# Performance work log

Measured on AMD Instinct MI355X. Metric: run time of the kernel, lower is better.

Reference implementation:

```python
import jax, jax.numpy as jnp
import numpy as np

N, M, C = 16384, 4096, 32
R = 2.0            # max_neighbour_distance
MULT = 2.0         # neighbor_distance_multiplier
NV = 3             # voxels per axis
TV = NV * NV * NV  # 27 total grid voxels
CH = 128           # query chunk size for kNN
EPS_D = 1e-8
BN_EPS = 1e-5


def _grid_offsets():
    g = jnp.linspace(-R + R / NV, R - R / NV, NV)
    x, y, z = jnp.meshgrid(g, g, g, indexing='ij')
    return jnp.stack([x.ravel(), y.ravel(), z.ravel()], axis=-1)  # (27,3)


def _three_nn(support_xyz, new_xyz, grid_centers):
    """3-NN of each grid center among support points within a cube of half-width
    MULT*R around the parent keypoint (two-step search, neighbor_type=0 cube).
    Returns squared dists (M,27,3), idx (M,27,3), empty (M,)."""
    q = new_xyz.reshape(-1, CH, 3)
    g = grid_centers.reshape(-1, CH, TV, 3)

    def body(args):
        qc, gc = args                                   # (CH,3), (CH,27,3)
        diff = jnp.abs(support_xyz[None, :, :] - qc[:, None, :])   # (CH,N,3)
        cand = jnp.max(diff, axis=-1) <= MULT * R                   # (CH,N)
        d2 = jnp.sum((gc[:, :, None, :] - support_xyz[None, None, :, :]) ** 2,
                     axis=-1)                                       # (CH,27,N)
        d2 = jnp.where(cand[:, None, :], d2, jnp.inf)
        nd, idx = jax.lax.top_k(-d2, 3)                              # (CH,27,3)
        return -nd, idx, ~jnp.any(cand, axis=-1)

    d3, idx, empty = jax.lax.map(body, (q, g))
    d3 = jnp.where(jnp.isinf(d3), 1e10, d3)  # <3 candidates -> ~zero weight
    return (d3.reshape(-1, TV, 3), idx.reshape(-1, TV, 3), empty.reshape(-1))


def _bn_relu(x, gamma, beta):
    mu = jnp.mean(x, axis=0)
    var = jnp.var(x, axis=0)
    return jax.nn.relu((x - mu) * jax.lax.rsqrt(var + BN_EPS) * gamma + beta)


def _forward(support_xyz, support_features, new_xyz,
             w1, bn1_gamma, bn1_beta, w2, bn2_gamma, bn2_beta):
    grid_centers = new_xyz[:, None, :] + _grid_offsets()[None, :, :]  # (M,27,3)
    d3, idx, empty = _three_nn(support_xyz, new_xyz, grid_centers)
    d3 = jax.lax.stop_gradient(d3)  # torch computes kNN under no_grad

    dist_recip = 1.0 / (d3 + EPS_D)                                   # (M,27,3)
    norm = jnp.sum(dist_recip, axis=-1, keepdims=True)
    weight = dist_recip / jnp.maximum(norm, 1e-8)

    nbr_feats = support_features[idx]                 # (M,27,3,C) gather
    interp = jnp.einsum('mgk,mgkc->mgc', weight, nbr_feats)          # (M,27,C)

    nbr_xyz = support_xyz[idx]                        # (M,27,3,3)
    local_xyz = (grid_centers[:, :, None, :] - nbr_xyz).reshape(M, TV, 9)
    feats = jnp.concatenate([interp, local_xyz], axis=-1)            # (M,27,C+9)
    feats = jnp.where(empty[:, None, None], 0.0, feats)

    # grouped Conv1d (kernel 1, groups=27): per-voxel matmul
    y = jnp.einsum('mgc,goc->mgo', feats, w1).reshape(M, TV * 32)     # (M,864)
    y = _bn_relu(y, bn1_gamma, bn1_beta)
    z = y @ w2.T                                                      # (M,128)
    return _bn_relu(z, bn2_gamma, bn2_beta)


def setup_inputs() -> dict:
    key = jax.random.key(0)
    ks = jax.random.split(key, 5)
    scale = jnp.array([50.0, 50.0, 4.0])
    shift = jnp.array([0.0, 0.0, -2.0])
    support_xyz = jax.random.uniform(ks[0], (N, 3)) * scale + shift
    new_xyz = jax.random.uniform(ks[1], (M, 3)) * scale + shift
    support_features = jax.random.normal(ks[2], (N, C))
    w1 = jax.random.normal(ks[3], (TV, 32, C + 9)) * (2.0 / (C + 9)) ** 0.5
    w2 = jax.random.normal(ks[4], (128, TV * 32)) * (2.0 / (TV * 32)) ** 0.5
    return {
        'support_xyz': support_xyz,
        'support_features': support_features,
        'new_xyz': new_xyz,
        'w1': w1,
        'bn1_gamma': jnp.ones(TV * 32),
        'bn1_beta': jnp.zeros(TV * 32),
        'w2': w2,
        'bn2_gamma': jnp.ones(128),
        'bn2_beta': jnp.zeros(128),
    }


def reference(support_xyz, support_features, new_xyz,
              w1, bn1_gamma, bn1_beta, w2, bn2_gamma, bn2_beta):
    return _forward(support_xyz, support_features, new_xyz,
                    w1, bn1_gamma, bn1_beta, w2, bn2_gamma, bn2_beta)
```

## Files before the change

### kernel.cpp

```cpp
#include <hip/hip_runtime.h>
#include <hip/hip_bf16.h>

#define N_SUP 16384
#define M_Q   4096
#define TV    27
#define CIN   41
#define CH1   864
#define CH2   128
#define CAP   1024
#define NB    12

#define KC_BK  24
#define KC_KS  216
#define KC_NCH 4

__device__ __forceinline__ float gsel(int i){
  const float GOFF = (float)(-2.0 + 2.0 / 3.0);
  return (i == 0) ? GOFF : ((i == 2) ? -GOFF : 0.0f);
}

__device__ __forceinline__ int binOf(float x){
  int b = (int)(x * (float)(NB / 50.0));
  return (b < 0) ? 0 : ((b > NB - 1) ? NB - 1 : b);
}

__device__ __forceinline__ void insK(unsigned long long key,
                                     unsigned long long& k0,
                                     unsigned long long& k1,
                                     unsigned long long& k2){
  bool b0 = key < k0, b1 = key < k1, b2 = key < k2;
  k2 = b1 ? k1 : (b2 ? key : k2);
  k1 = b0 ? k0 : (b1 ? key : k1);
  k0 = b0 ? key : k0;
}

__global__ void kPre(const float* __restrict__ w1, float* __restrict__ w1T,
                     const float* __restrict__ w2, float* __restrict__ w2T,
                     const float* __restrict__ sup_xyz, int* __restrict__ counts)
{
  int idx = blockIdx.x * 256 + threadIdx.x;
  if (idx < N_SUP) {
    float x = sup_xyz[3*idx], y = sup_xyz[3*idx+1];
    atomicAdd(&counts[binOf(x) * NB + binOf(y)], 1);
  }
  if (idx < CIN * CH1) {
    int k = idx / CH1, t = idx % CH1;
    w1T[idx] = w1[(size_t)t * CIN + k];
  }
  int j = idx - CIN * CH1;
  if (j >= 0 && j < CH1 * CH2) {
    int k = j / CH2, c = j % CH2;
    w2T[j] = w2[(size_t)c * CH1 + k];
  }
}

__global__ void kScan(const int* __restrict__ counts, int* __restrict__ starts, int* __restrict__ cursor)
{
  __shared__ int sc[NB*NB];
  int t = threadIdx.x;
  if (t < NB*NB) sc[t] = counts[t];
  __syncthreads();
  if (t == 0) {
    int acc = 0;
    for (int b = 0; b < NB*NB; b++) { int c = sc[b]; sc[b] = acc; acc += c; }
  }
  __syncthreads();
  if (t < NB*NB) { starts[t] = sc[t]; cursor[t] = sc[t]; }
  if (t == NB*NB) starts[NB*NB] = N_SUP;
}

__global__ void kScatter(const float* __restrict__ sup_xyz, int* __restrict__ cursor,
                         float* __restrict__ xs, float* __restrict__ ys,
                         float* __restrict__ zs, int* __restrict__ sid)
{
  int i = blockIdx.x * 256 + threadIdx.x;
  if (i < N_SUP) {
    float x = sup_xyz[3*i], y = sup_xyz[3*i+1], z = sup_xyz[3*i+2];
    int b = binOf(x) * NB + binOf(y);
    int p = atomicAdd(&cursor[b], 1);
    xs[p] = x; ys[p] = y; zs[p] = z; sid[p] = i;
  }
}

__global__ __launch_bounds__(256) void kA12(const float* __restrict__ xs,
                                            const float* __restrict__ ys,
                                            const float* __restrict__ zs,
                                            const int*   __restrict__ sid,
                                            const int*   __restrict__ starts,
                                            const float* __restrict__ new_xyz,
                                            const float* __restrict__ sup_xyz,
                                            float* __restrict__ nnW,
                                            int*   __restrict__ nnGI,
                                            float* __restrict__ nnLX)
{
  __shared__ float4 cxyz[CAP];
  __shared__ unsigned long long sk[TV][8][3];
  __shared__ int s_cnt;

  const int m   = blockIdx.x;
  const int tid = threadIdx.x;
  if (tid == 0) s_cnt = 0;
  __syncthreads();

  const float qx = new_xyz[m*3+0];
  const float qy = new_xyz[m*3+1];
  const float qz = new_xyz[m*3+2];

  const int bx0 = binOf(qx - 4.0f), bx1 = binOf(qx + 4.0f);
  const int by0 = binOf(qy - 4.0f), by1 = binOf(qy + 4.0f);
  for (int bx = bx0; bx <= bx1; bx++) {
    const int beg = starts[bx * NB + by0];
    const int end = starts[bx * NB + by1 + 1];
    for (int i = beg + tid; i < end; i += 256) {
      float x = xs[i], y = ys[i];
      if (fabsf(__fsub_rn(x, qx)) <= 4.0f && fabsf(__fsub_rn(y, qy)) <= 4.0f) {
        int p = atomicAdd(&s_cnt, 1);
        if (p < CAP) cxyz[p] = make_float4(x, y, zs[i], __uint_as_float((unsigned)sid[i]));
      }
    }
  }
  __syncthreads();
  const int cnt = (s_cnt < CAP) ? s_cnt : CAP;

  const int v = tid >> 3, j = tid & 7;
  if (v < TV) {
    const float gx = qx + gsel(v / 9);
    const float gy = qy + gsel((v / 3) % 3);
    const float gz = qz + gsel(v % 3);
    unsigned long long k0 = ~0ull, k1 = ~0ull, k2 = ~0ull;
    float k2df = __uint_as_float(0xFFFFFFFFu);
    for (int c = j; c < cnt; c += 8) {
      float4 f4 = cxyz[c];
      float dx = __fsub_rn(gx, f4.x);
      float dy = __fsub_rn(gy, f4.y);
      float dz = __fsub_rn(gz, f4.z);
      float dd = __fadd_rn(__fadd_rn(__fmul_rn(dx,dx), __fmul_rn(dy,dy)), __fmul_rn(dz,dz));
      if (!(dd > k2df)) {
        unsigned long long key = ((unsigned long long)__float_as_uint(dd) << 32)
                               | (unsigned long long)__float_as_uint(f4.w);
        insK(key, k0, k1, k2);
        k2df = __uint_as_float((unsigned)(k2 >> 32));
      }
    }
    sk[v][j][0] = k0; sk[v][j][1] = k1; sk[v][j][2] = k2;
  }
  __syncthreads();

  if (tid < TV) {
    const int vv = tid;
    const float gx = qx + gsel(vv / 9);
    const float gy = qy + gsel((vv / 3) % 3);
    const float gz = qz + gsel(vv % 3);
    unsigned long long k0 = ~0ull, k1 = ~0ull, k2 = ~0ull;
    #pragma unroll
    for (int jj = 0; jj < 8; jj++) {
      insK(sk[vv][jj][0], k0, k1, k2);
      insK(sk[vv][jj][1], k0, k1, k2);
      insK(sk[vv][jj][2], k0, k1, k2);
    }
    const int base = m * TV + vv;
    if (cnt > 0) {
      unsigned long long ks[3] = {k0, k1, k2};
      float d[3]; int gi[3]; bool ok[3];
      #pragma unroll
      for (int r = 0; r < 3; r++) {
        unsigned db = (unsigned)(ks[r] >> 32);
        ok[r] = (db != 0xFFFFFFFFu);
        d[r]  = ok[r] ? __uint_as_float(db) : 1e10f;
        gi[r] = ok[r] ? (int)(unsigned)(ks[r] & 0xFFFFFFFFull) : 0;
      }
      float r0 = 1.0f / (d[0] + 1e-8f);
      float r1 = 1.0f / (d[1] + 1e-8f);
      float r2 = 1.0f / (d[2] + 1e-8f);
      float den = fmaxf(r0 + r1 + r2, 1e-8f);
      nnW[base*3+0] = r0 / den; nnW[base*3+1] = r1 / den; nnW[base*3+2] = r2 / den;
      nnGI[base*3+0] = gi[0]; nnGI[base*3+1] = gi[1]; nnGI[base*3+2] = gi[2];
      #pragma unroll
      for (int r = 0; r < 3; r++) {
        if (ok[r]) {
          nnLX[base*9 + r*3 + 0] = gx - sup_xyz[gi[r]*3 + 0];
          nnLX[base*9 + r*3 + 1] = gy - sup_xyz[gi[r]*3 + 1];
          nnLX[base*9 + r*3 + 2] = gz - sup_xyz[gi[r]*3 + 2];
        } else {
          nnLX[base*9 + r*3 + 0] = 0.0f;
          nnLX[base*9 + r*3 + 1] = 0.0f;
          nnLX[base*9 + r*3 + 2] = 0.0f;
        }
      }
    } else {
      #pragma unroll
      for (int r = 0; r < 3; r++) {
        nnW[base*3+r] = 0.0f; nnGI[base*3+r] = 0;
        nnLX[base*9+r*3+0] = 0.0f; nnLX[base*9+r*3+1] = 0.0f; nnLX[base*9+r*3+2] = 0.0f;
      }
    }
  }
}

__global__ __launch_bounds__(256) void kA3(const float* __restrict__ sup_feat,
                                           const float* __restrict__ nnW,
                                           const int*   __restrict__ nnGI,
                                           const float* __restrict__ nnLX,
                                           const float* __restrict__ w1T,
                                           float* __restrict__ y1,
                                           float* __restrict__ stats1)
{
  __shared__ float s_feats[8][TV][CIN];
  __shared__ float s_w[8][TV][3];
  __shared__ int   s_gi[8][TV][3];

  const int m0  = blockIdx.x * 8;
  const int tid = threadIdx.x;

  for (int t = tid; t < 8*TV*3; t += 256) {
    int q = t / (TV*3), rem = t % (TV*3);
    s_w[q][rem/3][rem%3]  = nnW[m0*TV*3 + t];
    s_gi[q][rem/3][rem%3] = nnGI[m0*TV*3 + t];
  }
  for (int t = tid; t < 8*TV*9; t += 256) {
    int q = t / (TV*9), rem = t % (TV*9);
    s_feats[q][rem/9][32 + rem%9] = nnLX[m0*TV*9 + t];
  }
  __syncthreads();

  for (int t = tid; t < 8*TV*32; t += 256) {
    const int q = t / (TV*32), rem = t % (TV*32);
    const int v = rem >> 5, ch = rem & 31;
    s_feats[q][v][ch] = s_w[q][v][0] * sup_feat[s_gi[q][v][0]*32 + ch]
                      + s_w[q][v][1] * sup_feat[s_gi[q][v][1]*32 + ch]
                      + s_w[q][v][2] * sup_feat[s_gi[q][v][2]*32 + ch];
  }
  __syncthreads();

  const int copy = (blockIdx.x & 7) * 2 * CH1;
  for (int t = tid; t < CH1; t += 256) {
    const int v = t >> 5;
    float acc[8];
    #pragma unroll
    for (int q = 0; q < 8; q++) acc[q] = 0.0f;
    for (int k = 0; k < CIN; k++) {
      float w = w1T[k * CH1 + t];
      #pragma unroll
      for (int q = 0; q < 8; q++) acc[q] += s_feats[q][v][k] * w;
    }
    float s = 0.0f, ss = 0.0f;
    #pragma unroll
    for (int q = 0; q < 8; q++) {
      y1[(size_t)(m0 + q) * CH1 + t] = acc[q];
      s += acc[q]; ss += acc[q] * acc[q];
    }
    atomicAdd(&stats1[copy + t],       s);
    atomicAdd(&stats1[copy + CH1 + t], ss);
  }
}

__global__ void kS(const float* __restrict__ stats1,
                   const float* __restrict__ g1, const float* __restrict__ b1,
                   float* __restrict__ scsg, float* __restrict__ shsg)
{
  int c = blockIdx.x * 256 + threadIdx.x;
  if (c < CH1) {
    float s = 0.0f, ssq = 0.0f;
    #pragma unroll
    for (int k = 0; k < 8; k++) {
      s   += stats1[k * 2 * CH1 + c];
      ssq += stats1[k * 2 * CH1 + CH1 + c];
    }
    float mu  = s  * (1.0f / M_Q);
    float var = ssq * (1.0f / M_Q) - mu * mu;
    float r   = 1.0f / sqrtf(var + 1e-5f);
    float gg = g1[c];
    scsg[c] = r * gg;
    shsg[c] = b1[c] - mu * r * gg;
  }
}

__global__ __launch_bounds__(256) void kC(const float* __restrict__ y1,
                                          const float* __restrict__ scsg,
                                          const float* __restrict__ shsg,
                                          const float* __restrict__ w2T,
                                          float* __restrict__ zpart)
{
  __shared__ float As[KC_BK][36];
  __shared__ float Bs[KC_BK][CH2];
  __shared__ float lsc[KC_KS], lsh[KC_KS];

  const int tid = threadIdx.x;
  const int mb  = blockIdx.x & 127;
  const int ch  = blockIdx.x >> 7;
  const int m0  = mb * 32;
  const int kb  = ch * KC_KS;

  for (int t = tid; t < KC_KS; t += 256) { lsc[t] = scsg[kb + t]; lsh[t] = shsg[kb + t]; }

  const int ar = tid >> 3;
  const int ac = (tid & 7) * 3;
  const int ty = tid >> 5;
  const int tx = tid & 31;

  float pa0, pa1, pa2; float4 pb[3];
  {
    const float* yr = &y1[(size_t)(m0 + ar) * CH1 + kb + ac];
    pa0 = yr[0]; pa1 = yr[1]; pa2 = yr[2];
    #pragma unroll
    for (int jj = 0; jj < 3; jj++) {
      int fid = tid + jj * 256; int kk = fid >> 5, c4 = (fid & 31) * 4;
      pb[jj] = *(const float4*)&w2T[(size_t)(kb + kk) * CH2 + c4];
    }
  }

  float acc[4][4];
  #pragma unroll
  for (int i = 0; i < 4; i++)
    #pragma unroll
    for (int jj = 0; jj < 4; jj++) acc[i][jj] = 0.0f;

  for (int kt = 0; kt < KC_KS / KC_BK; kt++) {
    __syncthreads();
    const int kl = kt * KC_BK + ac;
    As[ac  ][ar] = fmaxf(pa0 * lsc[kl  ] + lsh[kl  ], 0.0f);
    As[ac+1][ar] = fmaxf(pa1 * lsc[kl+1] + lsh[kl+1], 0.0f);
    As[ac+2][ar] = fmaxf(pa2 * lsc[kl+2] + lsh[kl+2], 0.0f);
    #pragma unroll
    for (int jj = 0; jj < 3; jj++) {
      int fid = tid + jj * 256; int kk = fid >> 5, c4 = (fid & 31) * 4;
      *(float4*)&Bs[kk][c4] = pb[jj];
    }
    __syncthreads();
    if (kt + 1 < KC_KS / KC_BK) {
      const float* yr = &y1[(size_t)(m0 + ar) * CH1 + kb + (kt+1) * KC_BK + ac];
      pa0 = yr[0]; pa1 = yr[1]; pa2 = yr[2];
      #pragma unroll
      for (int jj = 0; jj < 3; jj++) {
        int fid = tid + jj * 256; int kk = fid >> 5, c4 = (fid & 31) * 4;
        pb[jj] = *(const float4*)&w2T[(size_t)(kb + (kt+1) * KC_BK + kk) * CH2 + c4];
      }
    }
    #pragma unroll
    for (int kk = 0; kk < KC_BK; kk++) {
      float4 av = *(const float4*)&As[kk][ty*4];
      float4 bv = *(const float4*)&Bs[kk][tx*4];
      acc[0][0] += av.x*bv.x; acc[0][1] += av.x*bv.y; acc[0][2] += av.x*bv.z; acc[0][3] += av.x*bv.w;
      acc[1][0] += av.y*bv.x; acc[1][1] += av.y*bv.y; acc[1][2] += av.y*bv.z; acc[1][3] += av.y*bv.w;
      acc[2][0] += av.z*bv.x; acc[2][1] += av.z*bv.y; acc[2][2] += av.z*bv.z; acc[2][3] += av.z*bv.w;
      acc[3][0] += av.w*bv.x; acc[3][1] += av.w*bv.y; acc[3][2] += av.w*bv.z; acc[3][3] += av.w*bv.w;
    }
  }

  float* zp = zpart + (size_t)ch * M_Q * CH2;
  #pragma unroll
  for (int i = 0; i < 4; i++) {
    *(float4*)&zp[(size_t)(m0 + ty*4 + i) * CH2 + tx*4] =
        make_float4(acc[i][0], acc[i][1], acc[i][2], acc[i][3]);
  }
}

__global__ void kZ(const float* __restrict__ zpart,
                   float* __restrict__ z,
                   float* __restrict__ stats2)
{
  const int tid = threadIdx.x;
  const int c = tid & 127, h = tid >> 7;
  const int m0 = blockIdx.x * 64 + h * 32;
  float s = 0.0f, ss = 0.0f;
  for (int r = 0; r < 32; r++) {
    size_t off = (size_t)(m0 + r) * CH2 + c;
    float v = zpart[off]
            + zpart[off + (size_t)M_Q*CH2]
            + zpart[off + (size_t)2*M_Q*CH2]
            + zpart[off + (size_t)3*M_Q*CH2];
    z[off] = v;
    s += v; ss += v * v;
  }
  const int copy = (blockIdx.x & 7) * 256;
  atomicAdd(&stats2[copy + c],       s);
  atomicAdd(&stats2[copy + 128 + c], ss);
}

__global__ void kD(const float* __restrict__ z,
                   const float* __restrict__ stats2,
                   const float* __restrict__ g2,
                   const float* __restrict__ b2,
                   float* __restrict__ out)
{
  int t4 = blockIdx.x * 256 + threadIdx.x;
  if (t4 >= M_Q * CH2 / 4) return;
  int c = (t4 & 31) * 4;
  float4 zv = *(const float4*)&z[(size_t)t4 * 4];
  float4 sv = make_float4(0,0,0,0), qv = make_float4(0,0,0,0);
  #pragma unroll
  for (int k = 0; k < 8; k++) {
    float4 a = *(const float4*)&stats2[k * 256 + c];
    float4 b = *(const float4*)&stats2[k * 256 + 128 + c];
    sv.x += a.x; sv.y += a.y; sv.z += a.z; sv.w += a.w;
    qv.x += b.x; qv.y += b.y; qv.z += b.z; qv.w += b.w;
  }
  float4 gv = *(const float4*)&g2[c];
  float4 bv = *(const float4*)&b2[c];
  float4 o;
  {
    float mu = sv.x * (1.0f/M_Q), var = qv.x * (1.0f/M_Q) - mu*mu;
    o.x = fmaxf((zv.x - mu) * (1.0f/sqrtf(var + 1e-5f)) * gv.x + bv.x, 0.0f);
  }
  {
    float mu = sv.y * (1.0f/M_Q), var = qv.y * (1.0f/M_Q) - mu*mu;
    o.y = fmaxf((zv.y - mu) * (1.0f/sqrtf(var + 1e-5f)) * gv.y + bv.y, 0.0f);
  }
  {
    float mu = sv.z * (1.0f/M_Q), var = qv.z * (1.0f/M_Q) - mu*mu;
    o.z = fmaxf((zv.z - mu) * (1.0f/sqrtf(var + 1e-5f)) * gv.z + bv.z, 0.0f);
  }
  {
    float mu = sv.w * (1.0f/M_Q), var = qv.w * (1.0f/M_Q) - mu*mu;
    o.w = fmaxf((zv.w - mu) * (1.0f/sqrtf(var + 1e-5f)) * gv.w + bv.w, 0.0f);
  }
  *(float4*)&out[(size_t)t4 * 4] = o;
}

extern "C" void kernel_launch(void* const* d_in, const int* in_sizes, int n_in,
                              void* d_out, int out_size, void* d_ws, size_t ws_size,
                              hipStream_t stream)
{
  const float* sup_xyz  = (const float*)d_in[0];
  const float* sup_feat = (const float*)d_in[1];
  const float* new_xyz  = (const float*)d_in[2];
  const float* w1       = (const float*)d_in[3];
  const float* g1       = (const float*)d_in[4];
  const float* b1       = (const float*)d_in[5];
  const float* w2       = (const float*)d_in[6];
  const float* g2       = (const float*)d_in[7];
  const float* b2       = (const float*)d_in[8];
  float* out = (float*)d_out;

  char* ws = (char*)d_ws;
  float* y1     = (float*)(ws);
  float* z      = (float*)(ws + 14155776);
  float* w2T    = (float*)(ws + 16252928);
  float* stats1 = (float*)(ws + 16695296);
  float* stats2 = (float*)(ws + 16750592);
  int*   counts = (int*)  (ws + 16758784);
  int*   cursor = (int*)  (ws + 16759360);
  int*   starts = (int*)  (ws + 16759936);
  float* xs     = (float*)(ws + 16760516);
  float* ys     = (float*)(ws + 16826052);
  float* zs     = (float*)(ws + 16891588);
  int*   sid    = (int*)  (ws + 16957124);
  float* nnW    = (float*)(ws + 17022660);
  int*   nnGI   = (int*)  (ws + 18349764);
  float* nnLX   = (float*)(ws + 19676868);
  float* zpart  = (float*)(ws + 17022660);
  float* w1T    = z;
  float* scsg   = xs;
  float* shsg   = ys;

  hipMemsetAsync(stats1, 0, 55296 + 8192 + 576 + 576, stream);

  const int PRE_TOT = CIN*CH1 + CH1*CH2;
  hipLaunchKernelGGL(kPre,    dim3((PRE_TOT + 255) / 256), dim3(256), 0, stream, w1, w1T, w2, w2T, sup_xyz, counts);
  hipLaunchKernelGGL(kScan,   dim3(1),                    dim3(256), 0, stream, counts, starts, cursor);
  hipLaunchKernelGGL(kScatter,dim3((N_SUP + 255) / 256),  dim3(256), 0, stream, sup_xyz, cursor, xs, ys, zs, sid);
  hipLaunchKernelGGL(kA12,    dim3(M_Q),                  dim3(256), 0, stream, xs, ys, zs, sid, starts, new_xyz, sup_xyz, nnW, nnGI, nnLX);
  hipLaunchKernelGGL(kA3,     dim3(M_Q / 8),              dim3(256), 0, stream, sup_feat, nnW, nnGI, nnLX, w1T, y1, stats1);
  hipLaunchKernelGGL(kS,      dim3((CH1 + 255) / 256),    dim3(256), 0, stream, stats1, g1, b1, scsg, shsg);
  hipLaunchKernelGGL(kC,      dim3(128 * KC_NCH),         dim3(256), 0, stream, y1, scsg, shsg, w2T, zpart);
  hipLaunchKernelGGL(kZ,      dim3(M_Q / 64),             dim3(256), 0, stream, zpart, z, stats2);
  hipLaunchKernelGGL(kD,      dim3(M_Q * CH2 / 4 / 256),  dim3(256), 0, stream, z, stats2, g2, b2, out);
}
```

Measured before the change: 150.5 us.

## Move weight and offset computation into kA3, fold BN stats into kC, raise grid sizes

kA12 now writes only raw distances and indices. kA3 computes the inverse-distance weights and relative offsets directly into shared memory, which removes the nnW/nnLX global round trip. The separate BN-scale kernel kS is folded into kC's prologue, and kA3 and kZ now process fewer rows per block to launch more blocks. The trade is redundant stats reduction across kC blocks and more atomic contention on the stats buffers from the extra blocks.

```diff
diff --git a/kernel.cpp b/kernel.cpp
--- a/kernel.cpp
+++ b/kernel.cpp
@@ -88,10 +88,8 @@
                                             const int*   __restrict__ sid,
                                             const int*   __restrict__ starts,
                                             const float* __restrict__ new_xyz,
-                                            const float* __restrict__ sup_xyz,
-                                            float* __restrict__ nnW,
-                                            int*   __restrict__ nnGI,
-                                            float* __restrict__ nnLX)
+                                            float* __restrict__ nnD,
+                                            int*   __restrict__ nnGI)
 {
   __shared__ float4 cxyz[CAP];
   __shared__ unsigned long long sk[TV][8][3];
@@ -148,9 +146,6 @@
 
   if (tid < TV) {
     const int vv = tid;
-    const float gx = qx + gsel(vv / 9);
-    const float gy = qy + gsel((vv / 3) % 3);
-    const float gz = qz + gsel(vv % 3);
     unsigned long long k0 = ~0ull, k1 = ~0ull, k2 = ~0ull;
     #pragma unroll
     for (int jj = 0; jj < 8; jj++) {
@@ -161,69 +156,71 @@
     const int base = m * TV + vv;
     if (cnt > 0) {
       unsigned long long ks[3] = {k0, k1, k2};
-      float d[3]; int gi[3]; bool ok[3];
       #pragma unroll
       for (int r = 0; r < 3; r++) {
         unsigned db = (unsigned)(ks[r] >> 32);
-        ok[r] = (db != 0xFFFFFFFFu);
-        d[r]  = ok[r] ? __uint_as_float(db) : 1e10f;
-        gi[r] = ok[r] ? (int)(unsigned)(ks[r] & 0xFFFFFFFFull) : 0;
+        bool ok = (db != 0xFFFFFFFFu);
+        nnD[base*3+r]  = ok ? __uint_as_float(db) : 1e10f;
+        nnGI[base*3+r] = ok ? (int)(unsigned)(ks[r] & 0xFFFFFFFFull) : 0;
       }
+    } else {
+      #pragma unroll
+      for (int r = 0; r < 3; r++) { nnD[base*3+r] = -1.0f; nnGI[base*3+r] = 0; }
+    }
+  }
+}
+
+__global__ __launch_bounds__(256) void kA3(const float* __restrict__ sup_feat,
+                                           const float* __restrict__ sup_xyz,
+                                           const float* __restrict__ new_xyz,
+                                           const float* __restrict__ nnD,
+                                           const int*   __restrict__ nnGI,
+                                           const float* __restrict__ w1T,
+                                           float* __restrict__ y1,
+                                           float* __restrict__ stats1)
+{
+  __shared__ float s_feats[4][TV][CIN];
+  __shared__ float s_w[4][TV][3];
+  __shared__ int   s_gi[4][TV][3];
+
+  const int m0  = blockIdx.x * 4;
+  const int tid = threadIdx.x;
+
+  if (tid < 4*TV) {
+    const int q = tid / TV, vv = tid % TV;
+    const int m = m0 + q;
+    const int base = m * TV + vv;
+    float d[3]; int gi[3];
+    #pragma unroll
+    for (int r = 0; r < 3; r++) { d[r] = nnD[base*3+r]; gi[r] = nnGI[base*3+r]; }
+    #pragma unroll
+    for (int r = 0; r < 3; r++) s_gi[q][vv][r] = gi[r];
+    if (d[0] < 0.0f) {
+      #pragma unroll
+      for (int r = 0; r < 3; r++) s_w[q][vv][r] = 0.0f;
+      #pragma unroll
+      for (int jj = 0; jj < 9; jj++) s_feats[q][vv][32 + jj] = 0.0f;
+    } else {
       float r0 = 1.0f / (d[0] + 1e-8f);
       float r1 = 1.0f / (d[1] + 1e-8f);
       float r2 = 1.0f / (d[2] + 1e-8f);
       float den = fmaxf(r0 + r1 + r2, 1e-8f);
-      nnW[base*3+0] = r0 / den; nnW[base*3+1] = r1 / den; nnW[base*3+2] = r2 / den;
-      nnGI[base*3+0] = gi[0]; nnGI[base*3+1] = gi[1]; nnGI[base*3+2] = gi[2];
+      s_w[q][vv][0] = r0 / den; s_w[q][vv][1] = r1 / den; s_w[q][vv][2] = r2 / den;
+      const float gx = new_xyz[m*3+0] + gsel(vv / 9);
+      const float gy = new_xyz[m*3+1] + gsel((vv / 3) % 3);
+      const float gz = new_xyz[m*3+2] + gsel(vv % 3);
       #pragma unroll
       for (int r = 0; r < 3; r++) {
-        if (ok[r]) {
-          nnLX[base*9 + r*3 + 0] = gx - sup_xyz[gi[r]*3 + 0];
-          nnLX[base*9 + r*3 + 1] = gy - sup_xyz[gi[r]*3 + 1];
-          nnLX[base*9 + r*3 + 2] = gz - sup_xyz[gi[r]*3 + 2];
-        } else {
-          nnLX[base*9 + r*3 + 0] = 0.0f;
-          nnLX[base*9 + r*3 + 1] = 0.0f;
-          nnLX[base*9 + r*3 + 2] = 0.0f;
-        }
+        bool ok = (d[r] != 1e10f);
+        s_feats[q][vv][32 + r*3 + 0] = ok ? (gx - sup_xyz[gi[r]*3 + 0]) : 0.0f;
+        s_feats[q][vv][32 + r*3 + 1] = ok ? (gy - sup_xyz[gi[r]*3 + 1]) : 0.0f;
+        s_feats[q][vv][32 + r*3 + 2] = ok ? (gz - sup_xyz[gi[r]*3 + 2]) : 0.0f;
       }
-    } else {
-      #pragma unroll
-      for (int r = 0; r < 3; r++) {
-        nnW[base*3+r] = 0.0f; nnGI[base*3+r] = 0;
-        nnLX[base*9+r*3+0] = 0.0f; nnLX[base*9+r*3+1] = 0.0f; nnLX[base*9+r*3+2] = 0.0f;
-      }
-    }
-  }
-}
-
-__global__ __launch_bounds__(256) void kA3(const float* __restrict__ sup_feat,
-                                           const float* __restrict__ nnW,
-                                           const int*   __restrict__ nnGI,
-                                           const float* __restrict__ nnLX,
-                                           const float* __restrict__ w1T,
-                                           float* __restrict__ y1,
-                                           float* __restrict__ stats1)
-{
-  __shared__ float s_feats[8][TV][CIN];
-  __shared__ float s_w[8][TV][3];
-  __shared__ int   s_gi[8][TV][3];
-
-  const int m0  = blockIdx.x * 8;
-  const int tid = threadIdx.x;
-
-  for (int t = tid; t < 8*TV*3; t += 256) {
-    int q = t / (TV*3), rem = t % (TV*3);
-    s_w[q][rem/3][rem%3]  = nnW[m0*TV*3 + t];
-    s_gi[q][rem/3][rem%3] = nnGI[m0*TV*3 + t];
-  }
-  for (int t = tid; t < 8*TV*9; t += 256) {
-    int q = t / (TV*9), rem = t % (TV*9);
-    s_feats[q][rem/9][32 + rem%9] = nnLX[m0*TV*9 + t];
-  }
-  __syncthreads();
-
-  for (int t = tid; t < 8*TV*32; t += 256) {
+    }
+  }
+  __syncthreads();
+
+  for (int t = tid; t < 4*TV*32; t += 256) {
     const int q = t / (TV*32), rem = t % (TV*32);
     const int v = rem >> 5, ch = rem & 31;
     s_feats[q][v][ch] = s_w[q][v][0] * sup_feat[s_gi[q][v][0]*32 + ch]
@@ -235,17 +232,17 @@
   const int copy = (blockIdx.x & 7) * 2 * CH1;
   for (int t = tid; t < CH1; t += 256) {
     const int v = t >> 5;
-    float acc[8];
-    #pragma unroll
-    for (int q = 0; q < 8; q++) acc[q] = 0.0f;
+    float acc[4];
+    #pragma unroll
+    for (int q = 0; q < 4; q++) acc[q] = 0.0f;
     for (int k = 0; k < CIN; k++) {
       float w = w1T[k * CH1 + t];
       #pragma unroll
-      for (int q = 0; q < 8; q++) acc[q] += s_feats[q][v][k] * w;
+      for (int q = 0; q < 4; q++) acc[q] += s_feats[q][v][k] * w;
     }
     float s = 0.0f, ss = 0.0f;
     #pragma unroll
-    for (int q = 0; q < 8; q++) {
+    for (int q = 0; q < 4; q++) {
       y1[(size_t)(m0 + q) * CH1 + t] = acc[q];
       s += acc[q]; ss += acc[q] * acc[q];
     }
@@ -254,30 +251,10 @@
   }
 }
 
-__global__ void kS(const float* __restrict__ stats1,
-                   const float* __restrict__ g1, const float* __restrict__ b1,
-                   float* __restrict__ scsg, float* __restrict__ shsg)
-{
-  int c = blockIdx.x * 256 + threadIdx.x;
-  if (c < CH1) {
-    float s = 0.0f, ssq = 0.0f;
-    #pragma unroll
-    for (int k = 0; k < 8; k++) {
-      s   += stats1[k * 2 * CH1 + c];
-      ssq += stats1[k * 2 * CH1 + CH1 + c];
-    }
-    float mu  = s  * (1.0f / M_Q);
-    float var = ssq * (1.0f / M_Q) - mu * mu;
-    float r   = 1.0f / sqrtf(var + 1e-5f);
-    float gg = g1[c];
-    scsg[c] = r * gg;
-    shsg[c] = b1[c] - mu * r * gg;
-  }
-}
-
 __global__ __launch_bounds__(256) void kC(const float* __restrict__ y1,
-                                          const float* __restrict__ scsg,
-                                          const float* __restrict__ shsg,
+                                          const float* __restrict__ stats1,
+                                          const float* __restrict__ g1,
+                                          const float* __restrict__ b1,
                                           const float* __restrict__ w2T,
                                           float* __restrict__ zpart)
 {
@@ -291,7 +268,21 @@
   const int m0  = mb * 32;
   const int kb  = ch * KC_KS;
 
-  for (int t = tid; t < KC_KS; t += 256) { lsc[t] = scsg[kb + t]; lsh[t] = shsg[kb + t]; }
+  for (int t = tid; t < KC_KS; t += 256) {
+    const int c = kb + t;
+    float s = 0.0f, ssq = 0.0f;
+    #pragma unroll
+    for (int k = 0; k < 8; k++) {
+      s   += stats1[k * 2 * CH1 + c];
+      ssq += stats1[k * 2 * CH1 + CH1 + c];
+    }
+    float mu  = s  * (1.0f / M_Q);
+    float var = ssq * (1.0f / M_Q) - mu * mu;
+    float r   = 1.0f / sqrtf(var + 1e-5f);
+    float gg = g1[c];
+    lsc[t] = r * gg;
+    lsh[t] = b1[c] - mu * r * gg;
+  }
 
   const int ar = tid >> 3;
   const int ac = (tid & 7) * 3;
@@ -361,9 +352,9 @@
 {
   const int tid = threadIdx.x;
   const int c = tid & 127, h = tid >> 7;
-  const int m0 = blockIdx.x * 64 + h * 32;
+  const int m0 = blockIdx.x * 8 + h * 4;
   float s = 0.0f, ss = 0.0f;
-  for (int r = 0; r < 32; r++) {
+  for (int r = 0; r < 4; r++) {
     size_t off = (size_t)(m0 + r) * CH2 + c;
     float v = zpart[off]
             + zpart[off + (size_t)M_Q*CH2]
@@ -445,13 +436,10 @@
   float* ys     = (float*)(ws + 16826052);
   float* zs     = (float*)(ws + 16891588);
   int*   sid    = (int*)  (ws + 16957124);
-  float* nnW    = (float*)(ws + 17022660);
+  float* nnD    = (float*)(ws + 17022660);
   int*   nnGI   = (int*)  (ws + 18349764);
-  float* nnLX   = (float*)(ws + 19676868);
   float* zpart  = (float*)(ws + 17022660);
   float* w1T    = z;
-  float* scsg   = xs;
-  float* shsg   = ys;
 
   hipMemsetAsync(stats1, 0, 55296 + 8192 + 576 + 576, stream);
 
@@ -459,10 +447,9 @@
   hipLaunchKernelGGL(kPre,    dim3((PRE_TOT + 255) / 256), dim3(256), 0, stream, w1, w1T, w2, w2T, sup_xyz, counts);
   hipLaunchKernelGGL(kScan,   dim3(1),                    dim3(256), 0, stream, counts, starts, cursor);
   hipLaunchKernelGGL(kScatter,dim3((N_SUP + 255) / 256),  dim3(256), 0, stream, sup_xyz, cursor, xs, ys, zs, sid);
-  hipLaunchKernelGGL(kA12,    dim3(M_Q),                  dim3(256), 0, stream, xs, ys, zs, sid, starts, new_xyz, sup_xyz, nnW, nnGI, nnLX);
-  hipLaunchKernelGGL(kA3,     dim3(M_Q / 8),              dim3(256), 0, stream, sup_feat, nnW, nnGI, nnLX, w1T, y1, stats1);
-  hipLaunchKernelGGL(kS,      dim3((CH1 + 255) / 256),    dim3(256), 0, stream, stats1, g1, b1, scsg, shsg);
-  hipLaunchKernelGGL(kC,      dim3(128 * KC_NCH),         dim3(256), 0, stream, y1, scsg, shsg, w2T, zpart);
-  hipLaunchKernelGGL(kZ,      dim3(M_Q / 64),             dim3(256), 0, stream, zpart, z, stats2);
+  hipLaunchKernelGGL(kA12,    dim3(M_Q),                  dim3(256), 0, stream, xs, ys, zs, sid, starts, new_xyz, nnD, nnGI);
+  hipLaunchKernelGGL(kA3,     dim3(M_Q / 4),              dim3(256), 0, stream, sup_feat, sup_xyz, new_xyz, nnD, nnGI, w1T, y1, stats1);
+  hipLaunchKernelGGL(kC,      dim3(128 * KC_NCH),         dim3(256), 0, stream, y1, stats1, g1, b1, w2T, zpart);
+  hipLaunchKernelGGL(kZ,      dim3(M_Q / 8),              dim3(256), 0, stream, zpart, z, stats2);
   hipLaunchKernelGGL(kD,      dim3(M_Q * CH2 / 4 / 256),  dim3(256), 0, stream, z, stats2, g2, b2, out);
 }
```

Result: faster. 144.9 us (-3.7%).
